# Kernel tuning notes

Hardware: AMD Instinct MI355X
Metric: run time of the kernel (lower is better)

Reference implementation:

```python
import jax, jax.numpy as jnp
import numpy as np

B, R, M, L, H = 256, 2048, 65536, 64, 4  # batch, reservoir, memory_size, key_len, read_heads


def setup_inputs() -> dict:
    key = jax.random.key(0)
    ks = jax.random.split(key, 4)
    s = 1.0 / np.sqrt(R).astype(np.float32)  # ~xavier scale for Linear weights
    return {
        "reservoir_state": jax.random.normal(ks[0], (B, R), dtype=jnp.float32),
        "memory": jax.random.normal(ks[1], (1, M, L), dtype=jnp.float32),
        "Wk": jax.random.normal(ks[2], (H * L, R), dtype=jnp.float32) * s,
        "bk": jnp.zeros((H * L,), dtype=jnp.float32),
        "Wb": jax.random.normal(ks[3], (H, R), dtype=jnp.float32) * s,
        "bb": jnp.zeros((H,), dtype=jnp.float32),
    }


def reference(reservoir_state, memory, Wk, bk, Wb, bb):
    b = reservoir_state.shape[0]
    h = Wb.shape[0]
    # key projection -> [B, H, L]
    keys = (reservoir_state @ Wk.T + bk).reshape(b, h, -1)
    # per-head key strength, relu-gated -> [B, H]
    betas = jax.nn.relu(reservoir_state @ Wb.T + bb)
    # content addressing: dot(keys, memory rows) -> [B, H, M]
    dots = jnp.einsum('bhl,ml->bhm', keys, memory[0])
    # normalize by key norm (as in original: sqrt(sum(keys^2)))
    dots = dots / jnp.sqrt(jnp.sum(keys ** 2, axis=-1, keepdims=True))
    # beta-scaled softmax over memory slots
    return jax.nn.softmax(betas[:, :, None] * dots, axis=-1)
```

## Files before the change

### kernel.cpp

```cpp
#include <hip/hip_runtime.h>
#include <hip/hip_bf16.h>

#define BB   256
#define RR   2048
#define MM   65536
#define LL   64
#define HH   4
#define NROW 1024
#define KEYS 256

typedef float f32x4 __attribute__((ext_vector_type(4)));
typedef short short8 __attribute__((ext_vector_type(8)));

#define MFMA(A,B,C) __builtin_amdgcn_mfma_f32_16x16x32_bf16((A),(B),(C),0,0,0)
#define LOG2E 1.4426950408889634f
#define EXP2F(x) __builtin_amdgcn_exp2f(x)

__device__ __forceinline__ unsigned short bf16_rn(float x) {
    union { float f; unsigned int u; } v; v.f = x;
    unsigned int r = v.u + 0x7FFFu + ((v.u >> 16) & 1u);
    return (unsigned short)(r >> 16);
}
__device__ __forceinline__ float bf16_to_f(unsigned short h) {
    union { float f; unsigned int u; } v; v.u = ((unsigned int)h) << 16; return v.f;
}
__device__ __forceinline__ void split8_store(const float* x, unsigned short* hi, unsigned short* lo) {
    unsigned int ph[4], pl[4];
#pragma unroll
    for (int j = 0; j < 4; ++j) {
        unsigned short h0 = bf16_rn(x[2*j]),   l0 = bf16_rn(x[2*j]   - bf16_to_f(h0));
        unsigned short h1 = bf16_rn(x[2*j+1]), l1 = bf16_rn(x[2*j+1] - bf16_to_f(h1));
        ph[j] = (unsigned int)h0 | ((unsigned int)h1 << 16);
        pl[j] = (unsigned int)l0 | ((unsigned int)l1 << 16);
    }
    ((uint4*)hi)[0] = make_uint4(ph[0], ph[1], ph[2], ph[3]);
    ((uint4*)lo)[0] = make_uint4(pl[0], pl[1], pl[2], pl[3]);
}

__global__ __launch_bounds__(256) void transpose_k(const float* __restrict__ in,
                                                   float* __restrict__ out,
                                                   int NR, int NC) {
    __shared__ float t[64 * 65];
    int r0 = blockIdx.x * 64, c0 = blockIdx.y * 64;
    int lane = threadIdx.x & 63, w = threadIdx.x >> 6;
#pragma unroll
    for (int i = 0; i < 16; ++i) {
        int rr = i * 4 + w;
        t[lane * 65 + rr] = in[(size_t)(r0 + rr) * NC + c0 + lane];
    }
    __syncthreads();
#pragma unroll
    for (int i = 0; i < 16; ++i) {
        int cc = i * 4 + w;
        out[(size_t)(c0 + cc) * NR + r0 + lane] = t[cc * 65 + lane];
    }
}

__global__ __launch_bounds__(256) void prep_mem(const float* __restrict__ mem,
                                                unsigned short* __restrict__ bhi,
                                                unsigned short* __restrict__ blo,
                                                float* __restrict__ normpart) {
    __shared__ float t[128 * 68];
    __shared__ float rowsq[128];
    int blk = blockIdx.x, tid = threadIdx.x;
    const f32x4* src = (const f32x4*)(mem + (size_t)blk * 128 * LL);
#pragma unroll
    for (int i = 0; i < 8; ++i) {
        int idx = i * 256 + tid;
        int row = idx >> 4, c4 = idx & 15;
        *(f32x4*)&t[row * 68 + c4 * 4] = src[idx];
    }
    __syncthreads();
    if (tid < 128) {
        const float* rp = t + tid * 68;
        float s = 0.f;
#pragma unroll
        for (int k = 0; k < 64; ++k) s = fmaf(rp[k], rp[k], s);
        rowsq[tid] = s;
    }
    __syncthreads();
    if (tid < 64) {
        float m = fmaxf(rowsq[tid], rowsq[tid + 64]);
#pragma unroll
        for (int off = 1; off < 64; off <<= 1) m = fmaxf(m, __shfl_xor(m, off, 64));
        if (tid == 0) normpart[blk] = m;
    }
#pragma unroll
    for (int i = 0; i < 4; ++i) {
        int slot = i * 256 + tid;
        int lane = slot & 63, frag_l = slot >> 6;
        int t_l = frag_l >> 1, c = frag_l & 1;
        int row = t_l * 16 + (lane & 15);
        int k0 = c * 32 + (lane >> 4) * 8;
        const float* p = t + row * 68 + k0;
        float x[8];
#pragma unroll
        for (int j = 0; j < 8; ++j) x[j] = p[j];
        size_t gslot = ((size_t)blk * 16 + frag_l) * 64 + lane;
        split8_store(x, bhi + gslot * 8, blo + gslot * 8);
    }
}

__global__ __launch_bounds__(256) void k0_keys(const float* __restrict__ S,
                                               const float* __restrict__ WkT,
                                               float* __restrict__ kpart) {
    __shared__ float sl[8 * 256];
    int bg = blockIdx.x, kc = blockIdx.y, tid = threadIdx.x;
    int b0 = bg * 8;
#pragma unroll
    for (int bi = 0; bi < 8; ++bi)
        sl[bi * 256 + tid] = S[(size_t)(b0 + bi) * RR + kc * 256 + tid];
    __syncthreads();
    float acc[8] = {0,0,0,0,0,0,0,0};
    const float* wp = WkT + (size_t)kc * 256 * KEYS + tid;
#pragma unroll 4
    for (int kk = 0; kk < 256; ++kk) {
        float wv = wp[kk * KEYS];
#pragma unroll
        for (int bi = 0; bi < 8; ++bi)
            acc[bi] = fmaf(sl[bi * 256 + kk], wv, acc[bi]);
    }
    float* op = kpart + (size_t)kc * BB * KEYS + (size_t)b0 * KEYS + tid;
#pragma unroll
    for (int bi = 0; bi < 8; ++bi)
        op[bi * KEYS] = acc[bi];
}

__global__ __launch_bounds__(256) void k1_finalize(const float* __restrict__ S,
                                                   const float* __restrict__ kpart,
                                                   const float* __restrict__ bk,
                                                   const float* __restrict__ Wb,
                                                   const float* __restrict__ bb,
                                                   const float* __restrict__ normpart,
                                                   float* __restrict__ q_rm,
                                                   float* __restrict__ brow) {
    int bh = blockIdx.x, b = bh >> 2, h = bh & 3;
    int tid = threadIdx.x, lane = tid & 63, w = tid >> 6;
    float p = 0.f;
#pragma unroll
    for (int i = 0; i < 8; ++i) {
        int k = i * 256 + tid;
        p += S[(size_t)b * RR + k] * Wb[(size_t)h * RR + k];
    }
    float nm = fmaxf(normpart[tid], normpart[256 + tid]);
#pragma unroll
    for (int off = 1; off < 64; off <<= 1) {
        p  += __shfl_xor(p, off, 64);
        nm  = fmaxf(nm, __shfl_xor(nm, off, 64));
    }
    __shared__ float red[4], redm[4];
    if (lane == 0) { red[w] = p; redm[w] = nm; }
    __syncthreads();
    if (tid < 64) {
        float beta = red[0] + red[1] + red[2] + red[3] + bb[h];
        beta = fmaxf(beta, 0.f);
        float maxn = sqrtf(fmaxf(fmaxf(redm[0], redm[1]), fmaxf(redm[2], redm[3])));
        float kv = bk[h * LL + lane];
#pragma unroll
        for (int c = 0; c < 8; ++c)
            kv += kpart[(size_t)c * BB * KEYS + (size_t)b * KEYS + h * LL + lane];
        float sq = kv * kv;
#pragma unroll
        for (int off = 1; off < 64; off <<= 1) sq += __shfl_xor(sq, off, 64);
        float scale = beta * LOG2E / sqrtf(sq);
        q_rm[(size_t)bh * LL + lane] = kv * scale;
        if (lane == 0) brow[bh] = beta * maxn * LOG2E;
    }
}

__global__ __launch_bounds__(256) void prep_a(const float* __restrict__ q_rm,
                                              unsigned short* __restrict__ ahi,
                                              unsigned short* __restrict__ alo) {
    int gid = blockIdx.x * 256 + threadIdx.x;
    int lane = gid & 63, frag = gid >> 6;
    int rtg = frag >> 1, c = frag & 1;
    int row = rtg * 16 + (lane & 15);
    int k0 = c * 32 + (lane >> 4) * 8;
    const float4* src = (const float4*)(q_rm + (size_t)row * LL + k0);
    float4 x0 = src[0], x1 = src[1];
    float x[8] = {x0.x, x0.y, x0.z, x0.w, x1.x, x1.y, x1.z, x1.w};
    split8_store(x, ahi + (size_t)gid * 8, alo + (size_t)gid * 8);
}

__device__ __forceinline__ void decode_wg(int bx, int& mblk, int& rg) {
    int wg = ((bx & 7) << 7) | (bx >> 3);
    mblk = wg >> 4; rg = wg & 15;
}

__global__ __launch_bounds__(256) void k2_mfma(const unsigned short* __restrict__ bhi,
                                               const unsigned short* __restrict__ blo,
                                               const unsigned short* __restrict__ ahi,
                                               const unsigned short* __restrict__ alo,
                                               const float* __restrict__ brow,
                                               float* __restrict__ psum) {
    int mblk, rg; decode_wg(blockIdx.x, mblk, rg);
    int tid = threadIdx.x, w = tid >> 6, lane = tid & 63;
    int g = lane >> 4;
    short8 Ah[4][2], Al[4][2];
#pragma unroll
    for (int rt = 0; rt < 4; ++rt)
#pragma unroll
        for (int c = 0; c < 2; ++c) {
            size_t off = ((size_t)((rg * 4 + rt) * 2 + c) * 64 + lane) * 8;
            Ah[rt][c] = *(const short8*)(ahi + off);
            Al[rt][c] = *(const short8*)(alo + off);
        }
    float br[4][4];
#pragma unroll
    for (int rt = 0; rt < 4; ++rt)
#pragma unroll
        for (int r = 0; r < 4; ++r)
            br[rt][r] = brow[rg * 64 + rt * 16 + g * 4 + r];
    float s[4][4] = {{0.f}};
    int t0 = mblk * 64 + w * 16;
    short8 Bh0, Bh1, Bl0, Bl1;
    {
        size_t o = (size_t)t0 * 1024 + (size_t)lane * 8;
        Bh0 = *(const short8*)(bhi + o); Bh1 = *(const short8*)(bhi + o + 512);
        Bl0 = *(const short8*)(blo + o); Bl1 = *(const short8*)(blo + o + 512);
    }
#pragma unroll 4
    for (int ti = 0; ti < 16; ++ti) {
        int tn = t0 + ((ti < 15) ? ti + 1 : 15);
        size_t on = (size_t)tn * 1024 + (size_t)lane * 8;
        short8 nh0 = *(const short8*)(bhi + on);
        short8 nh1 = *(const short8*)(bhi + on + 512);
        short8 nl0 = *(const short8*)(blo + on);
        short8 nl1 = *(const short8*)(blo + on + 512);
#pragma unroll
        for (int rt = 0; rt < 4; ++rt) {
            f32x4 C = {0.f, 0.f, 0.f, 0.f};
            C = MFMA(Ah[rt][0], Bh0, C);
            C = MFMA(Ah[rt][1], Bh1, C);
            C = MFMA(Al[rt][0], Bh0, C);
            C = MFMA(Al[rt][1], Bh1, C);
            C = MFMA(Ah[rt][0], Bl0, C);
            C = MFMA(Ah[rt][1], Bl1, C);
#pragma unroll
            for (int r = 0; r < 4; ++r)
                s[rt][r] += EXP2F(C[r] - br[rt][r]);
        }
        Bh0 = nh0; Bh1 = nh1; Bl0 = nl0; Bl1 = nl1;
    }
#pragma unroll
    for (int rt = 0; rt < 4; ++rt)
#pragma unroll
        for (int r = 0; r < 4; ++r) {
            float v = s[rt][r];
            v += __shfl_xor(v, 1, 64);
            v += __shfl_xor(v, 2, 64);
            v += __shfl_xor(v, 4, 64);
            v += __shfl_xor(v, 8, 64);
            s[rt][r] = v;
        }
    if ((lane & 15) == 0) {
        int col = mblk * 4 + w;
#pragma unroll
        for (int rt = 0; rt < 4; ++rt)
#pragma unroll
            for (int r = 0; r < 4; ++r) {
                int row = rg * 64 + rt * 16 + g * 4 + r;
                psum[(size_t)row * 256 + col] = s[rt][r];
            }
    }
}

__global__ __launch_bounds__(256) void k3_combine(const float* __restrict__ psum,
                                                  float* __restrict__ ginv) {
    int row = blockIdx.x, tid = threadIdx.x, lane = tid & 63, w = tid >> 6;
    float v = psum[(size_t)row * 256 + tid];
#pragma unroll
    for (int off = 1; off < 64; off <<= 1) v += __shfl_xor(v, off, 64);
    __shared__ float sm[4];
    if (lane == 0) sm[w] = v;
    __syncthreads();
    if (tid == 0) ginv[row] = 1.0f / (sm[0] + sm[1] + sm[2] + sm[3]);
}

__global__ __launch_bounds__(256) void k4_mfma(const unsigned short* __restrict__ bhi,
                                               const unsigned short* __restrict__ blo,
                                               const unsigned short* __restrict__ ahi,
                                               const unsigned short* __restrict__ alo,
                                               const float* __restrict__ brow,
                                               const float* __restrict__ ginv,
                                               float* __restrict__ out) {
    __shared__ float ot[16 * 516];
    int bx = blockIdx.x;
    int wg = ((bx & 7) << 7) | (bx >> 3);
    int mblk = wg >> 6, rg = wg & 63;
    int tid = threadIdx.x, w = tid >> 6, lane = tid & 63;
    int g = lane >> 4;
    short8 Ah[2], Al[2];
#pragma unroll
    for (int c = 0; c < 2; ++c) {
        size_t off = ((size_t)(rg * 2 + c) * 64 + lane) * 8;
        Ah[c] = *(const short8*)(ahi + off);
        Al[c] = *(const short8*)(alo + off);
    }
    float br[4], gv[4];
#pragma unroll
    for (int r = 0; r < 4; ++r) {
        int row = rg * 16 + g * 4 + r;
        br[r] = brow[row];
        gv[r] = ginv[row];
    }
    int tbase = mblk * 256 + w * 8;
    short8 Bh0, Bh1, Bl0, Bl1;
    {
        size_t o = (size_t)tbase * 1024 + (size_t)lane * 8;
        Bh0 = *(const short8*)(bhi + o); Bh1 = *(const short8*)(bhi + o + 512);
        Bl0 = *(const short8*)(blo + o); Bl1 = *(const short8*)(blo + o + 512);
    }
    for (int c = 0; c < 8; ++c) {
#pragma unroll
        for (int k = 0; k < 8; ++k) {
            int j = c * 8 + k;
            int jn = (j < 63) ? j + 1 : 63;
            int tn = tbase + (jn >> 3) * 32 + (jn & 7);
            size_t on = (size_t)tn * 1024 + (size_t)lane * 8;
            short8 nh0 = *(const short8*)(bhi + on);
            short8 nh1 = *(const short8*)(bhi + on + 512);
            short8 nl0 = *(const short8*)(blo + on);
            short8 nl1 = *(const short8*)(blo + on + 512);
            f32x4 C = {0.f, 0.f, 0.f, 0.f};
            C = MFMA(Ah[0], Bh0, C);
            C = MFMA(Ah[1], Bh1, C);
            C = MFMA(Al[0], Bh0, C);
            C = MFMA(Al[1], Bh1, C);
            C = MFMA(Ah[0], Bl0, C);
            C = MFMA(Ah[1], Bl1, C);
            int cbase = w * 128 + k * 16 + (lane & 15);
#pragma unroll
            for (int r = 0; r < 4; ++r)
                ot[(g * 4 + r) * 516 + cbase] = EXP2F(C[r] - br[r]) * gv[r];
            Bh0 = nh0; Bh1 = nh1; Bl0 = nl0; Bl1 = nl1;
        }
        __syncthreads();
        size_t gbase = (size_t)mblk * 4096 + (size_t)c * 512;
#pragma unroll
        for (int i = 0; i < 8; ++i) {
            int flat = i * 256 + tid;
            int rl = flat >> 7, slot = flat & 127;
            f32x4 v = *(const f32x4*)&ot[rl * 516 + slot * 4];
            float* dst = out + (size_t)(rg * 16 + rl) * MM + gbase + (size_t)slot * 4;
            __builtin_nontemporal_store(v, (f32x4*)dst);
        }
        __syncthreads();
    }
}

extern "C" void kernel_launch(void* const* d_in, const int* in_sizes, int n_in,
                              void* d_out, int out_size, void* d_ws, size_t ws_size,
                              hipStream_t stream) {
    const float* S   = (const float*)d_in[0];
    const float* mem = (const float*)d_in[1];
    const float* Wk  = (const float*)d_in[2];
    const float* bk  = (const float*)d_in[3];
    const float* Wb  = (const float*)d_in[4];
    const float* bb  = (const float*)d_in[5];
    float* out = (float*)d_out;

    float* WkT      = (float*)d_ws;
    float* kpart    = WkT   + (size_t)RR * KEYS;
    float* q_rm     = kpart + (size_t)8 * BB * KEYS;
    float* psum     = q_rm  + (size_t)NROW * LL;
    float* brow     = psum  + (size_t)NROW * 256;
    float* ginv     = brow  + NROW;
    float* normpart = ginv  + NROW;
    unsigned short* bhi = (unsigned short*)(normpart + 512);
    unsigned short* blo = bhi + (size_t)8192 * 512;
    unsigned short* ahi = blo + (size_t)8192 * 512;
    unsigned short* alo = ahi + (size_t)128 * 512;

    transpose_k<<<dim3(BB / 64, RR / 64), 256, 0, stream>>>(Wk, WkT, KEYS, RR);
    prep_mem   <<<512,         256, 0, stream>>>(mem, bhi, blo, normpart);
    k0_keys    <<<dim3(32, 8), 256, 0, stream>>>(S, WkT, kpart);
    k1_finalize<<<NROW,        256, 0, stream>>>(S, kpart, bk, Wb, bb, normpart, q_rm, brow);
    prep_a     <<<32,          256, 0, stream>>>(q_rm, ahi, alo);
    k2_mfma    <<<1024,        256, 0, stream>>>(bhi, blo, ahi, alo, brow, psum);
    k3_combine <<<NROW,        256, 0, stream>>>(psum, ginv);
    k4_mfma    <<<1024,        256, 0, stream>>>(bhi, blo, ahi, alo, brow, ginv, out);
}
```

Baseline: 355.4 us.

## Fuse small prep kernels to cut launch count from eight to four

The Wk transpose, memory preparation and key projection are merged into one setup kernel. Its key-projection blocks now transpose Wk through shared memory instead of reading a pre-transposed copy. The split of queries into bf16 hi/lo now happens in registers inside the MFMA kernels, and the row-sum reduction that produced ginv moves into the start of k4. This removes four launches and their intermediate buffers, at the cost of redundant query splitting and psum reduction per workgroup.

Result: no change. 359.4 us (+1.1%).

```diff
diff --git a/kernel.cpp b/kernel.cpp
--- a/kernel.cpp
+++ b/kernel.cpp
@@ -36,94 +36,102 @@
     ((uint4*)hi)[0] = make_uint4(ph[0], ph[1], ph[2], ph[3]);
     ((uint4*)lo)[0] = make_uint4(pl[0], pl[1], pl[2], pl[3]);
 }
-
-__global__ __launch_bounds__(256) void transpose_k(const float* __restrict__ in,
-                                                   float* __restrict__ out,
-                                                   int NR, int NC) {
-    __shared__ float t[64 * 65];
-    int r0 = blockIdx.x * 64, c0 = blockIdx.y * 64;
-    int lane = threadIdx.x & 63, w = threadIdx.x >> 6;
-#pragma unroll
-    for (int i = 0; i < 16; ++i) {
-        int rr = i * 4 + w;
-        t[lane * 65 + rr] = in[(size_t)(r0 + rr) * NC + c0 + lane];
-    }
-    __syncthreads();
-#pragma unroll
-    for (int i = 0; i < 16; ++i) {
-        int cc = i * 4 + w;
-        out[(size_t)(c0 + cc) * NR + r0 + lane] = t[cc * 65 + lane];
-    }
-}
-
-__global__ __launch_bounds__(256) void prep_mem(const float* __restrict__ mem,
-                                                unsigned short* __restrict__ bhi,
-                                                unsigned short* __restrict__ blo,
-                                                float* __restrict__ normpart) {
-    __shared__ float t[128 * 68];
-    __shared__ float rowsq[128];
-    int blk = blockIdx.x, tid = threadIdx.x;
-    const f32x4* src = (const f32x4*)(mem + (size_t)blk * 128 * LL);
-#pragma unroll
-    for (int i = 0; i < 8; ++i) {
-        int idx = i * 256 + tid;
-        int row = idx >> 4, c4 = idx & 15;
-        *(f32x4*)&t[row * 68 + c4 * 4] = src[idx];
-    }
-    __syncthreads();
-    if (tid < 128) {
-        const float* rp = t + tid * 68;
-        float s = 0.f;
-#pragma unroll
-        for (int k = 0; k < 64; ++k) s = fmaf(rp[k], rp[k], s);
-        rowsq[tid] = s;
-    }
-    __syncthreads();
-    if (tid < 64) {
-        float m = fmaxf(rowsq[tid], rowsq[tid + 64]);
-#pragma unroll
-        for (int off = 1; off < 64; off <<= 1) m = fmaxf(m, __shfl_xor(m, off, 64));
-        if (tid == 0) normpart[blk] = m;
-    }
-#pragma unroll
-    for (int i = 0; i < 4; ++i) {
-        int slot = i * 256 + tid;
-        int lane = slot & 63, frag_l = slot >> 6;
-        int t_l = frag_l >> 1, c = frag_l & 1;
-        int row = t_l * 16 + (lane & 15);
-        int k0 = c * 32 + (lane >> 4) * 8;
-        const float* p = t + row * 68 + k0;
-        float x[8];
-#pragma unroll
-        for (int j = 0; j < 8; ++j) x[j] = p[j];
-        size_t gslot = ((size_t)blk * 16 + frag_l) * 64 + lane;
-        split8_store(x, bhi + gslot * 8, blo + gslot * 8);
-    }
-}
-
-__global__ __launch_bounds__(256) void k0_keys(const float* __restrict__ S,
-                                               const float* __restrict__ WkT,
+__device__ __forceinline__ void split8_reg(const float* x, short8& hi, short8& lo) {
+    union { unsigned int u[4]; short8 s; } H, L;
+#pragma unroll
+    for (int j = 0; j < 4; ++j) {
+        unsigned short h0 = bf16_rn(x[2*j]),   l0 = bf16_rn(x[2*j]   - bf16_to_f(h0));
+        unsigned short h1 = bf16_rn(x[2*j+1]), l1 = bf16_rn(x[2*j+1] - bf16_to_f(h1));
+        H.u[j] = (unsigned int)h0 | ((unsigned int)h1 << 16);
+        L.u[j] = (unsigned int)l0 | ((unsigned int)l1 << 16);
+    }
+    hi = H.s; lo = L.s;
+}
+
+__global__ __launch_bounds__(256) void setup_k(const float* __restrict__ mem,
+                                               const float* __restrict__ Wk,
+                                               const float* __restrict__ S,
+                                               unsigned short* __restrict__ bhi,
+                                               unsigned short* __restrict__ blo,
+                                               float* __restrict__ normpart,
                                                float* __restrict__ kpart) {
-    __shared__ float sl[8 * 256];
-    int bg = blockIdx.x, kc = blockIdx.y, tid = threadIdx.x;
-    int b0 = bg * 8;
-#pragma unroll
-    for (int bi = 0; bi < 8; ++bi)
-        sl[bi * 256 + tid] = S[(size_t)(b0 + bi) * RR + kc * 256 + tid];
-    __syncthreads();
-    float acc[8] = {0,0,0,0,0,0,0,0};
-    const float* wp = WkT + (size_t)kc * 256 * KEYS + tid;
+    __shared__ float sh[18496];
+    int bx = blockIdx.x, tid = threadIdx.x;
+    if (bx < 512) {
+        float* t     = sh;
+        float* rowsq = sh + 128 * 68;
+        int blk = bx;
+        const f32x4* src = (const f32x4*)(mem + (size_t)blk * 128 * LL);
+#pragma unroll
+        for (int i = 0; i < 8; ++i) {
+            int idx = i * 256 + tid;
+            int row = idx >> 4, c4 = idx & 15;
+            *(f32x4*)&t[row * 68 + c4 * 4] = src[idx];
+        }
+        __syncthreads();
+        if (tid < 128) {
+            const float* rp = t + tid * 68;
+            float s = 0.f;
+#pragma unroll
+            for (int k = 0; k < 64; ++k) s = fmaf(rp[k], rp[k], s);
+            rowsq[tid] = s;
+        }
+        __syncthreads();
+        if (tid < 64) {
+            float m = fmaxf(rowsq[tid], rowsq[tid + 64]);
+#pragma unroll
+            for (int off = 1; off < 64; off <<= 1) m = fmaxf(m, __shfl_xor(m, off, 64));
+            if (tid == 0) normpart[blk] = m;
+        }
+#pragma unroll
+        for (int i = 0; i < 4; ++i) {
+            int slot = i * 256 + tid;
+            int lane = slot & 63, frag_l = slot >> 6;
+            int t_l = frag_l >> 1, c = frag_l & 1;
+            int row = t_l * 16 + (lane & 15);
+            int k0 = c * 32 + (lane >> 4) * 8;
+            const float* p = t + row * 68 + k0;
+            float x[8];
+#pragma unroll
+            for (int j = 0; j < 8; ++j) x[j] = p[j];
+            size_t gslot = ((size_t)blk * 16 + frag_l) * 64 + lane;
+            split8_store(x, bhi + gslot * 8, blo + gslot * 8);
+        }
+    } else {
+        float* sl = sh;
+        float* wk = sh + 2048;
+        int bx2 = bx - 512;
+        int bg = bx2 >> 3, kc = bx2 & 7;
+        int b0 = bg * 8;
+#pragma unroll
+        for (int bi = 0; bi < 8; ++bi)
+            sl[bi * 256 + tid] = S[(size_t)(b0 + bi) * RR + kc * 256 + tid];
+        float acc[8] = {0,0,0,0,0,0,0,0};
+        for (int sub = 0; sub < 4; ++sub) {
+            const f32x4* wsrc = (const f32x4*)(Wk + (size_t)tid * RR + kc * 256 + sub * 64);
+#pragma unroll
+            for (int i = 0; i < 16; ++i) {
+                f32x4 v = wsrc[i];
+#pragma unroll
+                for (int q = 0; q < 4; ++q)
+                    wk[(i * 4 + q) * 257 + tid] = v[q];
+            }
+            __syncthreads();
 #pragma unroll 4
-    for (int kk = 0; kk < 256; ++kk) {
-        float wv = wp[kk * KEYS];
+            for (int kkl = 0; kkl < 64; ++kkl) {
+                float wv = wk[kkl * 257 + tid];
+                int kk = sub * 64 + kkl;
+#pragma unroll
+                for (int bi = 0; bi < 8; ++bi)
+                    acc[bi] = fmaf(sl[bi * 256 + kk], wv, acc[bi]);
+            }
+            __syncthreads();
+        }
+        float* op = kpart + (size_t)kc * BB * KEYS + (size_t)b0 * KEYS + tid;
 #pragma unroll
         for (int bi = 0; bi < 8; ++bi)
-            acc[bi] = fmaf(sl[bi * 256 + kk], wv, acc[bi]);
-    }
-    float* op = kpart + (size_t)kc * BB * KEYS + (size_t)b0 * KEYS + tid;
-#pragma unroll
-    for (int bi = 0; bi < 8; ++bi)
-        op[bi * KEYS] = acc[bi];
+            op[bi * KEYS] = acc[bi];
+    }
 }
 
 __global__ __launch_bounds__(256) void k1_finalize(const float* __restrict__ S,
@@ -168,20 +176,6 @@
     }
 }
 
-__global__ __launch_bounds__(256) void prep_a(const float* __restrict__ q_rm,
-                                              unsigned short* __restrict__ ahi,
-                                              unsigned short* __restrict__ alo) {
-    int gid = blockIdx.x * 256 + threadIdx.x;
-    int lane = gid & 63, frag = gid >> 6;
-    int rtg = frag >> 1, c = frag & 1;
-    int row = rtg * 16 + (lane & 15);
-    int k0 = c * 32 + (lane >> 4) * 8;
-    const float4* src = (const float4*)(q_rm + (size_t)row * LL + k0);
-    float4 x0 = src[0], x1 = src[1];
-    float x[8] = {x0.x, x0.y, x0.z, x0.w, x1.x, x1.y, x1.z, x1.w};
-    split8_store(x, ahi + (size_t)gid * 8, alo + (size_t)gid * 8);
-}
-
 __device__ __forceinline__ void decode_wg(int bx, int& mblk, int& rg) {
     int wg = ((bx & 7) << 7) | (bx >> 3);
     mblk = wg >> 4; rg = wg & 15;
@@ -189,8 +183,7 @@
 
 __global__ __launch_bounds__(256) void k2_mfma(const unsigned short* __restrict__ bhi,
                                                const unsigned short* __restrict__ blo,
-                                               const unsigned short* __restrict__ ahi,
-                                               const unsigned short* __restrict__ alo,
+                                               const float* __restrict__ q_rm,
                                                const float* __restrict__ brow,
                                                float* __restrict__ psum) {
     int mblk, rg; decode_wg(blockIdx.x, mblk, rg);
@@ -201,9 +194,11 @@
     for (int rt = 0; rt < 4; ++rt)
 #pragma unroll
         for (int c = 0; c < 2; ++c) {
-            size_t off = ((size_t)((rg * 4 + rt) * 2 + c) * 64 + lane) * 8;
-            Ah[rt][c] = *(const short8*)(ahi + off);
-            Al[rt][c] = *(const short8*)(alo + off);
+            const float* qp = q_rm + (size_t)(rg * 64 + rt * 16 + (lane & 15)) * LL
+                              + c * 32 + (lane >> 4) * 8;
+            f32x4 x0 = *(const f32x4*)qp, x1 = *(const f32x4*)(qp + 4);
+            float x[8] = {x0[0], x0[1], x0[2], x0[3], x1[0], x1[1], x1[2], x1[3]};
+            split8_reg(x, Ah[rt][c], Al[rt][c]);
         }
     float br[4][4];
 #pragma unroll
@@ -265,44 +260,45 @@
     }
 }
 
-__global__ __launch_bounds__(256) void k3_combine(const float* __restrict__ psum,
-                                                  float* __restrict__ ginv) {
-    int row = blockIdx.x, tid = threadIdx.x, lane = tid & 63, w = tid >> 6;
-    float v = psum[(size_t)row * 256 + tid];
-#pragma unroll
-    for (int off = 1; off < 64; off <<= 1) v += __shfl_xor(v, off, 64);
-    __shared__ float sm[4];
-    if (lane == 0) sm[w] = v;
-    __syncthreads();
-    if (tid == 0) ginv[row] = 1.0f / (sm[0] + sm[1] + sm[2] + sm[3]);
-}
-
 __global__ __launch_bounds__(256) void k4_mfma(const unsigned short* __restrict__ bhi,
                                                const unsigned short* __restrict__ blo,
-                                               const unsigned short* __restrict__ ahi,
-                                               const unsigned short* __restrict__ alo,
+                                               const float* __restrict__ q_rm,
                                                const float* __restrict__ brow,
-                                               const float* __restrict__ ginv,
+                                               const float* __restrict__ psum,
                                                float* __restrict__ out) {
     __shared__ float ot[16 * 516];
+    __shared__ float gsh[16];
     int bx = blockIdx.x;
     int wg = ((bx & 7) << 7) | (bx >> 3);
     int mblk = wg >> 6, rg = wg & 63;
     int tid = threadIdx.x, w = tid >> 6, lane = tid & 63;
     int g = lane >> 4;
+    {
+        int row16 = tid >> 4, seg = tid & 15;
+        const float* pp = psum + (size_t)(rg * 16 + row16) * 256 + seg * 16;
+        float part = 0.f;
+#pragma unroll
+        for (int j = 0; j < 16; ++j) part += pp[j];
+#pragma unroll
+        for (int off = 1; off < 16; off <<= 1) part += __shfl_xor(part, off, 64);
+        if (seg == 0) gsh[row16] = 1.0f / part;
+    }
     short8 Ah[2], Al[2];
 #pragma unroll
     for (int c = 0; c < 2; ++c) {
-        size_t off = ((size_t)(rg * 2 + c) * 64 + lane) * 8;
-        Ah[c] = *(const short8*)(ahi + off);
-        Al[c] = *(const short8*)(alo + off);
-    }
+        const float* qp = q_rm + (size_t)(rg * 16 + (lane & 15)) * LL
+                          + c * 32 + (lane >> 4) * 8;
+        f32x4 x0 = *(const f32x4*)qp, x1 = *(const f32x4*)(qp + 4);
+        float x[8] = {x0[0], x0[1], x0[2], x0[3], x1[0], x1[1], x1[2], x1[3]};
+        split8_reg(x, Ah[c], Al[c]);
+    }
+    __syncthreads();
     float br[4], gv[4];
 #pragma unroll
     for (int r = 0; r < 4; ++r) {
         int row = rg * 16 + g * 4 + r;
         br[r] = brow[row];
-        gv[r] = ginv[row];
+        gv[r] = gsh[g * 4 + r];
     }
     int tbase = mblk * 256 + w * 8;
     short8 Bh0, Bh1, Bl0, Bl1;
@@ -360,24 +356,16 @@
     const float* bb  = (const float*)d_in[5];
     float* out = (float*)d_out;
 
-    float* WkT      = (float*)d_ws;
-    float* kpart    = WkT   + (size_t)RR * KEYS;
+    float* kpart    = (float*)d_ws;
     float* q_rm     = kpart + (size_t)8 * BB * KEYS;
     float* psum     = q_rm  + (size_t)NROW * LL;
     float* brow     = psum  + (size_t)NROW * 256;
-    float* ginv     = brow  + NROW;
-    float* normpart = ginv  + NROW;
+    float* normpart = brow  + NROW;
     unsigned short* bhi = (unsigned short*)(normpart + 512);
     unsigned short* blo = bhi + (size_t)8192 * 512;
-    unsigned short* ahi = blo + (size_t)8192 * 512;
-    unsigned short* alo = ahi + (size_t)128 * 512;
-
-    transpose_k<<<dim3(BB / 64, RR / 64), 256, 0, stream>>>(Wk, WkT, KEYS, RR);
-    prep_mem   <<<512,         256, 0, stream>>>(mem, bhi, blo, normpart);
-    k0_keys    <<<dim3(32, 8), 256, 0, stream>>>(S, WkT, kpart);
-    k1_finalize<<<NROW,        256, 0, stream>>>(S, kpart, bk, Wb, bb, normpart, q_rm, brow);
-    prep_a     <<<32,          256, 0, stream>>>(q_rm, ahi, alo);
-    k2_mfma    <<<1024,        256, 0, stream>>>(bhi, blo, ahi, alo, brow, psum);
-    k3_combine <<<NROW,        256, 0, stream>>>(psum, ginv);
-    k4_mfma    <<<1024,        256, 0, stream>>>(bhi, blo, ahi, alo, brow, ginv, out);
-}
+
+    setup_k    <<<768,  256, 0, stream>>>(mem, Wk, S, bhi, blo, normpart, kpart);
+    k1_finalize<<<NROW, 256, 0, stream>>>(S, kpart, bk, Wb, bb, normpart, q_rm, brow);
+    k2_mfma    <<<1024, 256, 0, stream>>>(bhi, blo, q_rm, brow, psum);
+    k4_mfma    <<<1024, 256, 0, stream>>>(bhi, blo, q_rm, brow, psum, out);
+}
```
